# Performance work log

Hardware: AMD Instinct MI355X
Metric: run time of the kernel (lower is better)

The kernel has to match this reference:

```python
import jax, jax.numpy as jnp
import numpy as np

HEADS = 8


def setup_inputs() -> dict:
    key = jax.random.key(0)
    k1, k2, k3, k4, k5, k6 = jax.random.split(key, 6)
    B, S, E = 2, 2048, 512
    D = E // HEADS
    return {
        "values": jax.random.normal(k1, (B, S, E), dtype=jnp.float32),
        "keys": jax.random.normal(k2, (B, S, E), dtype=jnp.float32),
        "queries": jax.random.normal(k3, (B, S, E), dtype=jnp.float32),
        "mask": jax.random.randint(k4, (B, 1, 1, S), 0, 2, dtype=jnp.int32),
        "W_v": jax.random.normal(k5, (D, D), dtype=jnp.float32) * (1.0 / np.sqrt(D)),
        "W_o": jax.random.normal(k6, (E, E), dtype=jnp.float32) * (1.0 / np.sqrt(E)),
        "b_o": jnp.zeros((E,), dtype=jnp.float32),
    }


def reference(values, keys, queries, mask, W_v, W_o, b_o):
    B, S, E = queries.shape
    H = HEADS
    D = E // H
    # reshape to (b, s, h, d) and apply the SAME W_v linear to v, k, q
    # (faithful to the original, which calls self.values on all three)
    v = jnp.einsum('bshd,ed->bshe', values.reshape(B, -1, H, D), W_v)
    k = jnp.einsum('bshd,ed->bshe', keys.reshape(B, -1, H, D), W_v)
    q = jnp.einsum('bshd,ed->bshe', queries.reshape(B, -1, H, D), W_v)
    # unscaled attention scores (original has no 1/sqrt(d))
    energy = jnp.einsum('bqhd,bkhd->bhqk', q, k)  # (b, h, q, k)
    energy = jnp.where(mask == 0, -jnp.inf, energy)
    attn = jax.nn.softmax(energy, axis=3)
    out = jnp.einsum('bhqk,bkhd->bqhd', attn, v)  # (b, q, h, d)
    out = out.reshape(B, S, E)
    return out @ W_o.T + b_o
```

## Files before the change

kernel.cpp:

```cpp
#include <hip/hip_runtime.h>


#define B_ 2
#define S_ 2048
#define E_ 512
#define H_ 8
#define D_ 64

typedef unsigned short ushort_t;
typedef __attribute__((ext_vector_type(8))) short short8;
typedef __attribute__((ext_vector_type(8))) _Float16 half8;
typedef __attribute__((ext_vector_type(4))) float f32x4;

__device__ __forceinline__ ushort_t f2bs(float x) {
    union { float f; unsigned int u; } a; a.f = x;
    unsigned int u = a.u;
    u += 0x7fffu + ((u >> 16) & 1u);
    return (ushort_t)(u >> 16);
}
__device__ __forceinline__ float bs2f(ushort_t h) {
    union { unsigned int u; float f; } a; a.u = ((unsigned int)h) << 16;
    return a.f;
}
__device__ __forceinline__ ushort_t f2hs(float x) {
    _Float16 h = (_Float16)x;
    ushort_t u; __builtin_memcpy(&u, &h, 2);
    return u;
}
__device__ __forceinline__ void split16(const float4* g, ushort_t* hi, ushort_t* lo) {
    #pragma unroll
    for (int q = 0; q < 4; ++q) {
        float4 f = g[q];
        float vv[4] = {f.x, f.y, f.z, f.w};
        #pragma unroll
        for (int j = 0; j < 4; ++j) {
            ushort_t h = f2bs(vv[j]);
            hi[q * 4 + j] = h;
            lo[q * 4 + j] = f2bs(vv[j] - bs2f(h));
        }
    }
}

__global__ void __launch_bounds__(256) proj_mfma(
    const float* __restrict__ quer, const float* __restrict__ keys,
    const float* __restrict__ vals, const float* __restrict__ Wv,
    ushort_t* __restrict__ qf, ushort_t* __restrict__ kf,
    ushort_t* __restrict__ vt)
{
    __shared__ ushort_t Ah[64 * 72], Al[64 * 72];
    __shared__ ushort_t Bh[64 * 72], Bl[64 * 72];
    const int tens = blockIdx.y;
    const float* src = tens == 0 ? quer : (tens == 1 ? keys : vals);
    const int bx = blockIdx.x;
    const int st = bx & 31, bh = bx >> 5;
    const int b = bh >> 3, h = bh & 7;
    const int s0 = st * 64;
    const int t = threadIdx.x;

    {
        int e = t >> 2, dg = (t & 3) * 16;
        ushort_t th[16], tl[16];
        split16((const float4*)(Wv + e * 64 + dg), th, tl);
        *(uint4*)&Bh[e * 72 + dg] = *(uint4*)th;  *(uint4*)&Bh[e * 72 + dg + 8] = *(uint4*)(th + 8);
        *(uint4*)&Bl[e * 72 + dg] = *(uint4*)tl;  *(uint4*)&Bl[e * 72 + dg + 8] = *(uint4*)(tl + 8);
    }
    {
        int row = t >> 2, cg = (t & 3) * 16;
        const float* g = src + ((size_t)b * S_ + s0 + row) * 512 + h * 64 + cg;
        ushort_t th[16], tl[16];
        split16((const float4*)g, th, tl);
        *(uint4*)&Ah[row * 72 + cg] = *(uint4*)th;  *(uint4*)&Ah[row * 72 + cg + 8] = *(uint4*)(th + 8);
        *(uint4*)&Al[row * 72 + cg] = *(uint4*)tl;  *(uint4*)&Al[row * 72 + cg + 8] = *(uint4*)(tl + 8);
    }
    __syncthreads();

    const int w = t >> 6, lm = t & 15, quad = (t >> 4) & 3;
    f32x4 acc[4];
    #pragma unroll
    for (int nt = 0; nt < 4; ++nt) acc[nt] = (f32x4){0.f, 0.f, 0.f, 0.f};

    #pragma unroll
    for (int kk = 0; kk < 2; ++kk) {
        short8 ah = *(const short8*)&Ah[(w * 16 + lm) * 72 + kk * 32 + quad * 8];
        short8 al = *(const short8*)&Al[(w * 16 + lm) * 72 + kk * 32 + quad * 8];
        #pragma unroll
        for (int nt = 0; nt < 4; ++nt) {
            short8 bh8 = *(const short8*)&Bh[(nt * 16 + lm) * 72 + kk * 32 + quad * 8];
            short8 bl8 = *(const short8*)&Bl[(nt * 16 + lm) * 72 + kk * 32 + quad * 8];
            acc[nt] = __builtin_amdgcn_mfma_f32_16x16x32_bf16(ah, bh8, acc[nt], 0, 0, 0);
            acc[nt] = __builtin_amdgcn_mfma_f32_16x16x32_bf16(al, bh8, acc[nt], 0, 0, 0);
            acc[nt] = __builtin_amdgcn_mfma_f32_16x16x32_bf16(ah, bl8, acc[nt], 0, 0, 0);
        }
    }

    if (tens < 2) {
        ushort_t* dst = tens == 0 ? qf : kf;
        #pragma unroll
        for (int nt = 0; nt < 4; ++nt) {
            #pragma unroll
            for (int r = 0; r < 4; ++r) {
                size_t addr = ((size_t)bh * S_ + s0 + w * 16 + quad * 4 + r) * 64 + nt * 16 + lm;
                dst[addr] = f2hs(acc[nt][r]);
            }
        }
    } else {
        #pragma unroll
        for (int nt = 0; nt < 4; ++nt) {
            unsigned int p0 = (unsigned int)f2bs(acc[nt][0]) | ((unsigned int)f2bs(acc[nt][1]) << 16);
            unsigned int p1 = (unsigned int)f2bs(acc[nt][2]) | ((unsigned int)f2bs(acc[nt][3]) << 16);
            uint2 pk; pk.x = p0; pk.y = p1;
            size_t addr = ((size_t)bh * 64 + nt * 16 + lm) * S_ + s0 + w * 16 + quad * 4;
            *(uint2*)&vt[addr] = pk;
        }
    }
}

__global__ void __launch_bounds__(256) attn_mfma(
    const ushort_t* __restrict__ qf, const ushort_t* __restrict__ kf,
    const ushort_t* __restrict__ vt, const int* __restrict__ mask,
    ushort_t* __restrict__ ctx)
{
    __shared__ ushort_t Ks[2][64 * 72];
    __shared__ ushort_t Vt[2][64 * 72];
    __shared__ ushort_t Ps[4 * 16 * 72];
    __shared__ float    mb[2][64];

    const int bx = blockIdx.x;
    const int qt = bx & 31;
    const int bh = bx >> 5;
    const int b  = bh >> 3;
    const int t  = threadIdx.x;
    const int w = t >> 6, lm = t & 15, quad = (t >> 4) & 3;
    const int q0 = qt * 64;
    const int wbase = w * 16 * 72;

    const int srow = t >> 2, scg = (t & 3) * 16;
    const size_t kgbase = ((size_t)bh * S_ + srow) * 64 + scg;
    const size_t vgbase = ((size_t)bh * 64 + srow) * S_ + scg;

    half8 aq[2];
    {
        size_t qrow = ((size_t)bh * S_ + q0 + w * 16 + lm) * 64 + quad * 8;
        aq[0] = *(const half8*)&qf[qrow];
        aq[1] = *(const half8*)&qf[qrow + 32];
    }
    short8 ones;
    #pragma unroll
    for (int j = 0; j < 8; ++j) ones[j] = (short)0x3F80;

    f32x4 acc[4];
    #pragma unroll
    for (int nt = 0; nt < 4; ++nt) acc[nt] = (f32x4){0.f, 0.f, 0.f, 0.f};
    f32x4 acc_l = (f32x4){0.f, 0.f, 0.f, 0.f};

    {
        *(uint4*)&Ks[0][srow * 72 + scg]     = *(const uint4*)&kf[kgbase];
        *(uint4*)&Ks[0][srow * 72 + scg + 8] = *(const uint4*)&kf[kgbase + 8];
        *(uint4*)&Vt[0][srow * 72 + scg]     = *(const uint4*)&vt[vgbase];
        *(uint4*)&Vt[0][srow * 72 + scg + 8] = *(const uint4*)&vt[vgbase + 8];
        if (t < 64) mb[0][t] = mask[b * S_ + t] ? -64.f : -1e30f;
    }
    __syncthreads();

    int cur = 0;
    for (int kc = 0; kc < S_ / 64; ++kc) {
        const bool pf = (kc + 1) < (S_ / 64);

        uint4 pk0, pk1, pv0, pv1; int mnext = 0;
        if (pf) {
            size_t ka = kgbase + (size_t)(kc + 1) * 64 * 64;
            pk0 = *(const uint4*)&kf[ka];
            pk1 = *(const uint4*)&kf[ka + 8];
            size_t va = vgbase + (size_t)(kc + 1) * 64;
            pv0 = *(const uint4*)&vt[va];
            pv1 = *(const uint4*)&vt[va + 8];
            if (t < 64) mnext = mask[b * S_ + (kc + 1) * 64 + t];
        }

        const ushort_t* Kc = Ks[cur];
        const ushort_t* Vc = Vt[cur];

        #pragma unroll
        for (int nt = 0; nt < 4; ++nt) {
            f32x4 s = (f32x4){0.f, 0.f, 0.f, 0.f};
            #pragma unroll
            for (int kk = 0; kk < 2; ++kk) {
                half8 ak = *(const half8*)&Kc[(nt * 16 + lm) * 72 + kk * 32 + quad * 8];
                s = __builtin_amdgcn_mfma_f32_16x16x32_f16(ak, aq[kk], s, 0, 0, 0);
            }
            f32x4 mv = *(const f32x4*)&mb[cur][nt * 16 + quad * 4];
            float p0 = __expf(s[0] + mv[0]);
            float p1 = __expf(s[1] + mv[1]);
            float p2 = __expf(s[2] + mv[2]);
            float p3 = __expf(s[3] + mv[3]);
            uint2 pkd;
            pkd.x = (unsigned int)f2bs(p0) | ((unsigned int)f2bs(p1) << 16);
            pkd.y = (unsigned int)f2bs(p2) | ((unsigned int)f2bs(p3) << 16);
            *(uint2*)&Ps[wbase + lm * 72 + nt * 16 + quad * 4] = pkd;
        }
        asm volatile("s_waitcnt lgkmcnt(0)" ::: "memory");

        #pragma unroll
        for (int kk = 0; kk < 2; ++kk) {
            short8 ap = *(const short8*)&Ps[wbase + lm * 72 + kk * 32 + quad * 8];
            #pragma unroll
            for (int nt = 0; nt < 4; ++nt) {
                short8 bv = *(const short8*)&Vc[(nt * 16 + lm) * 72 + kk * 32 + quad * 8];
                acc[nt] = __builtin_amdgcn_mfma_f32_16x16x32_bf16(ap, bv, acc[nt], 0, 0, 0);
            }
            acc_l = __builtin_amdgcn_mfma_f32_16x16x32_bf16(ap, ones, acc_l, 0, 0, 0);
        }

        if (pf) {
            const int nxt = cur ^ 1;
            *(uint4*)&Ks[nxt][srow * 72 + scg]     = pk0;
            *(uint4*)&Ks[nxt][srow * 72 + scg + 8] = pk1;
            *(uint4*)&Vt[nxt][srow * 72 + scg]     = pv0;
            *(uint4*)&Vt[nxt][srow * 72 + scg + 8] = pv1;
            if (t < 64) mb[nxt][t] = mnext ? -64.f : -1e30f;
            __syncthreads();
        }
        cur ^= 1;
    }

    const int h = bh & 7;
    #pragma unroll
    for (int r = 0; r < 4; ++r) {
        float inv = 1.f / acc_l[r];
        int s = q0 + w * 16 + quad * 4 + r;
        #pragma unroll
        for (int nt = 0; nt < 4; ++nt) {
            int d = nt * 16 + lm;
            ctx[((size_t)b * S_ + s) * E_ + h * D_ + d] = f2bs(acc[nt][r] * inv);
        }
    }
}

__global__ void __launch_bounds__(256) outproj_mfma(
    const ushort_t* __restrict__ ctx, const float* __restrict__ Wo,
    const float* __restrict__ bo, float* __restrict__ out)
{
    __shared__ ushort_t As[64 * 72];
    __shared__ ushort_t Bs[64 * 72];
    const int m0 = blockIdx.x * 64, n0 = blockIdx.y * 64;
    const int t = threadIdx.x;
    const int w = t >> 6, lm = t & 15, quad = (t >> 4) & 3;

    f32x4 acc[4];
    #pragma unroll
    for (int nt = 0; nt < 4; ++nt) acc[nt] = (f32x4){0.f, 0.f, 0.f, 0.f};

    for (int kc = 0; kc < E_ / 64; ++kc) {
        __syncthreads();
        {
            int row = t >> 2, cg = (t & 3) * 16;
            const ushort_t* g = ctx + (size_t)(m0 + row) * E_ + kc * 64 + cg;
            *(uint4*)&As[row * 72 + cg]     = *(const uint4*)g;
            *(uint4*)&As[row * 72 + cg + 8] = *(const uint4*)(g + 8);
        }
        {
            int n = t >> 2, kg = (t & 3) * 16;
            const float4* g = (const float4*)(Wo + (size_t)(n0 + n) * E_ + kc * 64 + kg);
            ushort_t tmp[16];
            #pragma unroll
            for (int q = 0; q < 4; ++q) {
                float4 f = g[q];
                tmp[q * 4 + 0] = f2bs(f.x); tmp[q * 4 + 1] = f2bs(f.y);
                tmp[q * 4 + 2] = f2bs(f.z); tmp[q * 4 + 3] = f2bs(f.w);
            }
            *(uint4*)&Bs[n * 72 + kg]     = *(uint4*)tmp;
            *(uint4*)&Bs[n * 72 + kg + 8] = *(uint4*)(tmp + 8);
        }
        __syncthreads();

        #pragma unroll
        for (int kk = 0; kk < 2; ++kk) {
            short8 a = *(const short8*)&As[(w * 16 + lm) * 72 + kk * 32 + quad * 8];
            #pragma unroll
            for (int nt = 0; nt < 4; ++nt) {
                short8 bb = *(const short8*)&Bs[(nt * 16 + lm) * 72 + kk * 32 + quad * 8];
                acc[nt] = __builtin_amdgcn_mfma_f32_16x16x32_bf16(a, bb, acc[nt], 0, 0, 0);
            }
        }
    }

    #pragma unroll
    for (int nt = 0; nt < 4; ++nt) {
        float bias = bo[n0 + nt * 16 + lm];
        #pragma unroll
        for (int r = 0; r < 4; ++r) {
            int m = m0 + w * 16 + quad * 4 + r;
            out[(size_t)m * E_ + n0 + nt * 16 + lm] = acc[nt][r] + bias;
        }
    }
}

extern "C" void kernel_launch(void* const* d_in, const int* in_sizes, int n_in,
                              void* d_out, int out_size, void* d_ws, size_t ws_size,
                              hipStream_t stream) {
    const float* vals = (const float*)d_in[0];
    const float* keys = (const float*)d_in[1];
    const float* quer = (const float*)d_in[2];
    const int*   mask = (const int*)d_in[3];
    const float* Wv   = (const float*)d_in[4];
    const float* Wo   = (const float*)d_in[5];
    const float* bo   = (const float*)d_in[6];
    float* out = (float*)d_out;

    const size_t N = (size_t)B_ * H_ * S_ * D_;
    ushort_t* ws  = (ushort_t*)d_ws;
    ushort_t* qf  = ws;
    ushort_t* kf  = ws + N;
    ushort_t* vt  = ws + 2 * N;
    ushort_t* ctx = ws + 3 * N;

    proj_mfma<<<dim3(B_ * H_ * (S_ / 64), 3), 256, 0, stream>>>(
        quer, keys, vals, Wv, qf, kf, vt);
    attn_mfma<<<B_ * H_ * (S_ / 64), 256, 0, stream>>>(qf, kf, vt, mask, ctx);
    outproj_mfma<<<dim3((B_ * S_) / 64, E_ / 64), 256, 0, stream>>>(ctx, Wo, bo, out);
}
```

Before: 140.1 us.

## Split attention key range across two wave groups with LDS reduction

The attention kernel grows from 256 to 512 threads. The second group of four waves processes the odd 64-key chunks while the first group takes the even chunks, so each iteration consumes 128 keys. Partial output and row-sum accumulators are then combined through shared memory before the first group writes the normalized context. The goal is more waves per query tile to hide latency and raise MFMA occupancy. In exchange it adds an extra barrier per iteration and a reduction epilogue.

```diff
diff --git a/kernel.cpp b/kernel.cpp
--- a/kernel.cpp
+++ b/kernel.cpp
@@ -115,14 +115,14 @@
     }
 }
 
-__global__ void __launch_bounds__(256) attn_mfma(
+__global__ void __launch_bounds__(512, 4) attn_mfma(
     const ushort_t* __restrict__ qf, const ushort_t* __restrict__ kf,
     const ushort_t* __restrict__ vt, const int* __restrict__ mask,
     ushort_t* __restrict__ ctx)
 {
     __shared__ ushort_t Ks[2][64 * 72];
     __shared__ ushort_t Vt[2][64 * 72];
-    __shared__ ushort_t Ps[4 * 16 * 72];
+    __shared__ ushort_t Ps[8 * 16 * 72];
     __shared__ float    mb[2][64];
 
     const int bx = blockIdx.x;
@@ -130,17 +130,21 @@
     const int bh = bx >> 5;
     const int b  = bh >> 3;
     const int t  = threadIdx.x;
-    const int w = t >> 6, lm = t & 15, quad = (t >> 4) & 3;
+    const int w  = t >> 6;
+    const int wq = w & 3;
+    const int ws = w >> 2;
+    const int lm = t & 15, quad = (t >> 4) & 3;
     const int q0 = qt * 64;
     const int wbase = w * 16 * 72;
 
-    const int srow = t >> 2, scg = (t & 3) * 16;
+    const int srow = t >> 3;
+    const int scg  = (t & 7) * 8;
     const size_t kgbase = ((size_t)bh * S_ + srow) * 64 + scg;
     const size_t vgbase = ((size_t)bh * 64 + srow) * S_ + scg;
 
     half8 aq[2];
     {
-        size_t qrow = ((size_t)bh * S_ + q0 + w * 16 + lm) * 64 + quad * 8;
+        size_t qrow = ((size_t)bh * S_ + q0 + wq * 16 + lm) * 64 + quad * 8;
         aq[0] = *(const half8*)&qf[qrow];
         aq[1] = *(const half8*)&qf[qrow + 32];
     }
@@ -154,31 +158,30 @@
     f32x4 acc_l = (f32x4){0.f, 0.f, 0.f, 0.f};
 
     {
-        *(uint4*)&Ks[0][srow * 72 + scg]     = *(const uint4*)&kf[kgbase];
-        *(uint4*)&Ks[0][srow * 72 + scg + 8] = *(const uint4*)&kf[kgbase + 8];
-        *(uint4*)&Vt[0][srow * 72 + scg]     = *(const uint4*)&vt[vgbase];
-        *(uint4*)&Vt[0][srow * 72 + scg + 8] = *(const uint4*)&vt[vgbase + 8];
-        if (t < 64) mb[0][t] = mask[b * S_ + t] ? -64.f : -1e30f;
-    }
-    __syncthreads();
-
-    int cur = 0;
-    for (int kc = 0; kc < S_ / 64; ++kc) {
-        const bool pf = (kc + 1) < (S_ / 64);
-
-        uint4 pk0, pk1, pv0, pv1; int mnext = 0;
+        *(uint4*)&Ks[0][srow * 72 + scg] = *(const uint4*)&kf[kgbase];
+        *(uint4*)&Ks[1][srow * 72 + scg] = *(const uint4*)&kf[kgbase + 4096];
+        *(uint4*)&Vt[0][srow * 72 + scg] = *(const uint4*)&vt[vgbase];
+        *(uint4*)&Vt[1][srow * 72 + scg] = *(const uint4*)&vt[vgbase + 64];
+        if (t < 128) mb[t >> 6][t & 63] = mask[b * S_ + t] ? -64.f : -1e30f;
+    }
+    __syncthreads();
+
+    for (int is = 0; is < S_ / 128; ++is) {
+        const bool pf = (is + 1) < (S_ / 128);
+
+        uint4 pk0, pk1, pv0, pv1; int mnx = 0;
         if (pf) {
-            size_t ka = kgbase + (size_t)(kc + 1) * 64 * 64;
-            pk0 = *(const uint4*)&kf[ka];
-            pk1 = *(const uint4*)&kf[ka + 8];
-            size_t va = vgbase + (size_t)(kc + 1) * 64;
-            pv0 = *(const uint4*)&vt[va];
-            pv1 = *(const uint4*)&vt[va + 8];
-            if (t < 64) mnext = mask[b * S_ + (kc + 1) * 64 + t];
-        }
-
-        const ushort_t* Kc = Ks[cur];
-        const ushort_t* Vc = Vt[cur];
+            size_t ko = kgbase + (size_t)(2 * (is + 1)) * 4096;
+            pk0 = *(const uint4*)&kf[ko];
+            pk1 = *(const uint4*)&kf[ko + 4096];
+            size_t vo = vgbase + (size_t)(2 * (is + 1)) * 64;
+            pv0 = *(const uint4*)&vt[vo];
+            pv1 = *(const uint4*)&vt[vo + 64];
+            if (t < 128) mnx = mask[b * S_ + (2 * (is + 1)) * 64 + t];
+        }
+
+        const ushort_t* Kc = Ks[ws];
+        const ushort_t* Vc = Vt[ws];
 
         #pragma unroll
         for (int nt = 0; nt < 4; ++nt) {
@@ -188,7 +191,7 @@
                 half8 ak = *(const half8*)&Kc[(nt * 16 + lm) * 72 + kk * 32 + quad * 8];
                 s = __builtin_amdgcn_mfma_f32_16x16x32_f16(ak, aq[kk], s, 0, 0, 0);
             }
-            f32x4 mv = *(const f32x4*)&mb[cur][nt * 16 + quad * 4];
+            f32x4 mv = *(const f32x4*)&mb[ws][nt * 16 + quad * 4];
             float p0 = __expf(s[0] + mv[0]);
             float p1 = __expf(s[1] + mv[1]);
             float p2 = __expf(s[2] + mv[2]);
@@ -199,6 +202,7 @@
             *(uint2*)&Ps[wbase + lm * 72 + nt * 16 + quad * 4] = pkd;
         }
         asm volatile("s_waitcnt lgkmcnt(0)" ::: "memory");
+        __builtin_amdgcn_sched_barrier(0);
 
         #pragma unroll
         for (int kk = 0; kk < 2; ++kk) {
@@ -211,27 +215,62 @@
             acc_l = __builtin_amdgcn_mfma_f32_16x16x32_bf16(ap, ones, acc_l, 0, 0, 0);
         }
 
+        __syncthreads();
         if (pf) {
-            const int nxt = cur ^ 1;
-            *(uint4*)&Ks[nxt][srow * 72 + scg]     = pk0;
-            *(uint4*)&Ks[nxt][srow * 72 + scg + 8] = pk1;
-            *(uint4*)&Vt[nxt][srow * 72 + scg]     = pv0;
-            *(uint4*)&Vt[nxt][srow * 72 + scg + 8] = pv1;
-            if (t < 64) mb[nxt][t] = mnext ? -64.f : -1e30f;
+            *(uint4*)&Ks[0][srow * 72 + scg] = pk0;
+            *(uint4*)&Ks[1][srow * 72 + scg] = pk1;
+            *(uint4*)&Vt[0][srow * 72 + scg] = pv0;
+            *(uint4*)&Vt[1][srow * 72 + scg] = pv1;
+            if (t < 128) mb[t >> 6][t & 63] = mnx ? -64.f : -1e30f;
             __syncthreads();
         }
-        cur ^= 1;
-    }
-
-    const int h = bh & 7;
-    #pragma unroll
-    for (int r = 0; r < 4; ++r) {
-        float inv = 1.f / acc_l[r];
-        int s = q0 + w * 16 + quad * 4 + r;
-        #pragma unroll
-        for (int nt = 0; nt < 4; ++nt) {
-            int d = nt * 16 + lm;
-            ctx[((size_t)b * S_ + s) * E_ + h * D_ + d] = f2bs(acc[nt][r] * inv);
+    }
+
+    float* cf = (float*)Ps;
+    const int lane = t & 63;
+    __syncthreads();
+    if (ws == 1) {
+        const int base = (wq * 64 + lane) * 18;
+        #pragma unroll
+        for (int nt = 0; nt < 4; ++nt) {
+            #pragma unroll
+            for (int r = 0; r < 4; r += 2) {
+                float2 v2; v2.x = acc[nt][r]; v2.y = acc[nt][r + 1];
+                *(float2*)&cf[base + nt * 4 + r] = v2;
+            }
+        }
+    }
+    __syncthreads();
+    if (ws == 0) {
+        const int base = (wq * 64 + lane) * 18;
+        #pragma unroll
+        for (int nt = 0; nt < 4; ++nt) {
+            #pragma unroll
+            for (int r = 0; r < 4; ++r) acc[nt][r] += cf[base + nt * 4 + r];
+        }
+    }
+    __syncthreads();
+    if (ws == 1) {
+        const int base = (wq * 64 + lane) * 5;
+        #pragma unroll
+        for (int r = 0; r < 4; ++r) cf[base + r] = acc_l[r];
+    }
+    __syncthreads();
+
+    if (ws == 0) {
+        const int base = (wq * 64 + lane) * 5;
+        #pragma unroll
+        for (int r = 0; r < 4; ++r) acc_l[r] += cf[base + r];
+        const int h = bh & 7;
+        #pragma unroll
+        for (int r = 0; r < 4; ++r) {
+            float inv = 1.f / acc_l[r];
+            int s = q0 + wq * 16 + quad * 4 + r;
+            #pragma unroll
+            for (int nt = 0; nt < 4; ++nt) {
+                int d = nt * 16 + lm;
+                ctx[((size_t)b * S_ + s) * E_ + h * D_ + d] = f2bs(acc[nt][r] * inv);
+            }
         }
     }
 }
@@ -316,6 +355,6 @@
 
     proj_mfma<<<dim3(B_ * H_ * (S_ / 64), 3), 256, 0, stream>>>(
         quer, keys, vals, Wv, qf, kf, vt);
-    attn_mfma<<<B_ * H_ * (S_ / 64), 256, 0, stream>>>(qf, kf, vt, mask, ctx);
+    attn_mfma<<<B_ * H_ * (S_ / 64), 512, 0, stream>>>(qf, kf, vt, mask, ctx);
     outproj_mfma<<<dim3((B_ * S_) / 64, E_ / 64), 256, 0, stream>>>(ctx, Wo, bo, out);
 }
```

Result: faster. 132.0 us (-5.8%).
